# Performance work log

Hardware: AMD Instinct MI355X
Metric: run time of the kernel (lower is better)

Reference implementation:

```python
import jax, jax.numpy as jnp
import numpy as np
import math

B = 128        # batch (= bipartite matching N)
L = 16         # detector layers (MAX_LAYER)
E = 768        # n_embd
D = E // 2     # RFF target_dim
H = 12         # n_head
HD = E // H    # head_size
NL = 6         # n_layer
SEQ = 12       # tokens after concats: 3+3 -> 6 -> +currentLayer -> 12
MAX_LAYER = L
LN_EPS = 1e-3  # keras LayerNormalization default


def setup_inputs() -> dict:
    key = jax.random.key(0)
    ks = jax.random.split(key, 8)
    inp = {}
    inp["X"] = jax.random.normal(ks[0], (B, L, 3), dtype=jnp.float32) * 50.0
    inp["targets"] = jax.random.normal(ks[1], (B, L, 3), dtype=jnp.float32)
    # RandomFourierFeatures params (random per-call in original; fixed here):
    # x: xmin=-160,xmax=160,n=9*1024 ; y: n=12*512 ; dE: xmin=0,xmax=230,n=2300
    specs = [(-160.0, 160.0, 9 * 1024), (-160.0, 160.0, 12 * 512), (0.0, 230.0, 2300)]
    om, ph = [], []
    for i, (xmin, xmax, n) in enumerate(specs):
        k1, k2 = jax.random.split(jax.random.fold_in(ks[2], i))
        omin = 2.0 * math.pi / (xmax - xmin)
        lo, hi = math.log(omin / n), math.log(omin)
        om.append(jnp.exp(jax.random.uniform(k1, (D,), minval=lo, maxval=hi)))
        ph.append(jax.random.uniform(k2, (D,)))  # B ~ U(0,1)*scale, scale=1
    inp["omegas"] = jnp.stack(om).astype(jnp.float32)  # (3, D)
    inp["phases"] = jnp.stack(ph).astype(jnp.float32)  # (3, D)
    # np.random.permutation per layer-step, fixed here
    inp["perms"] = jnp.stack(
        [jax.random.permutation(jax.random.fold_in(ks[3], i), B) for i in range(L - 1)]
    ).astype(jnp.int32)  # (L-1, B)
    # transformer weights (stacked over layers)
    kk = jax.random.split(ks[4], 16)
    s = 0.02
    inp["Wq"] = jax.random.normal(kk[0], (NL, E, H, HD)) * s
    inp["bq"] = jnp.zeros((NL, H, HD))
    inp["Wk"] = jax.random.normal(kk[1], (NL, E, H, HD)) * s
    inp["bk"] = jnp.zeros((NL, H, HD))
    inp["Wv"] = jax.random.normal(kk[2], (NL, E, H, HD)) * s
    inp["bv"] = jnp.zeros((NL, H, HD))
    inp["Wo"] = jax.random.normal(kk[3], (NL, H, HD, E)) * s
    inp["bo"] = jnp.zeros((NL, E))
    inp["ln1g"] = jnp.ones((NL, E)); inp["ln1b"] = jnp.zeros((NL, E))
    inp["ln2g"] = jnp.ones((NL, E)); inp["ln2b"] = jnp.zeros((NL, E))
    inp["W1"] = jax.random.normal(kk[4], (NL, E, 4 * E)) * s
    inp["b1f"] = jnp.zeros((NL, 4 * E))
    inp["W2"] = jax.random.normal(kk[5], (NL, 4 * E, E)) * s
    inp["b2f"] = jnp.zeros((NL, E))
    inp["lnfg"] = jnp.ones((E,)); inp["lnfb"] = jnp.zeros((E,))
    inp["Wout"] = jax.random.normal(kk[6], (SEQ * E, 3)) * s
    inp["bout"] = jnp.zeros((3,))
    return inp


def _ln(x, g, b):
    mu = jnp.mean(x, -1, keepdims=True)
    v = jnp.var(x, -1, keepdims=True)
    return (x - mu) * jax.lax.rsqrt(v + LN_EPS) * g + b


def _greedy_match(cost):
    """Greedy bipartite matching: sort all NxN costs ascending, assign first-come.
    Returns row_to_col_match_vec (N,) int32."""
    N = cost.shape[0]
    order = jnp.argsort(cost.reshape(-1))

    def step(carry, k):
        row, col = carry
        i = k // N
        j = k % N
        ok = (row[i] == -1) & (col[j] == -1)
        row = row.at[i].set(jnp.where(ok, j, row[i]))
        col = col.at[j].set(jnp.where(ok, i, col[j]))
        return (row, col), None

    init = (jnp.full((N,), -1, jnp.int32), jnp.full((N,), -1, jnp.int32))
    (row, _), _ = jax.lax.scan(step, init, order)
    return row


def _forward(X, targets, omegas, phases, perms, Wq, bq, Wk, bk, Wv, bv, Wo, bo,
             ln1g, ln1b, ln2g, ln2b, W1, b1f, W2, b2f, lnfg, lnfb, Wout, bout):
    # RFF: (B,L,3) -> (B,L,3,D)
    XS = jnp.cos(X[..., None] * omegas[None, None, :, :] + phases[None, None, :, :])
    losses = []
    scale = 1.0 / math.sqrt(HD)
    for lidx in range(1, L):
        xc = XS[:, -lidx]        # (B,3,D)
        xp = XS[:, -lidx - 1]    # (B,3,D)
        x = jnp.concatenate([xc, xp], axis=2)            # (B,3,E)
        y = targets[:, -lidx + 1]                        # (B,3)
        y_prev = jnp.broadcast_to(y[:, :, None], (B, 3, E))
        x = jnp.concatenate([x, y_prev], axis=1)         # (B,6,E)
        cur = jnp.full_like(x, float(MAX_LAYER - lidx))
        x = jnp.concatenate([x, cur], axis=1)            # (B,12,E)
        x = x[perms[lidx - 1]]                           # batch permutation
        for l in range(NL):
            h = _ln(x, ln1g[l], ln1b[l])
            q = jnp.einsum('bse,ehd->bshd', h, Wq[l]) + bq[l]
            k = jnp.einsum('bse,ehd->bshd', h, Wk[l]) + bk[l]
            v = jnp.einsum('bse,ehd->bshd', h, Wv[l]) + bv[l]
            att = jax.nn.softmax(jnp.einsum('bqhd,bkhd->bhqk', q, k) * scale, axis=-1)
            o = jnp.einsum('bhqk,bkhd->bqhd', att, v)
            x = x + (jnp.einsum('bqhd,hde->bqe', o, Wo[l]) + bo[l])
            h = _ln(x, ln2g[l], ln2b[l])
            x = x + (jnp.maximum(h @ W1[l] + b1f[l], 0.0) @ W2[l] + b2f[l])
        x = _ln(x, lnfg, lnfb).reshape(B, SEQ * E)
        logits = x @ Wout + bout                         # (B,3)
        tgt = targets[:, -lidx]                          # (B,3)
        cost = jnp.sqrt(jnp.sum((logits[:, None, :] - tgt[None, :, :]) ** 2, axis=-1) + 1e-12)
        m = _greedy_match(jax.lax.stop_gradient(cost))
        lm = logits[m]                                   # gather per original
        losses.append(jnp.mean((lm - tgt) ** 2))
    return jnp.mean(jnp.stack(losses))


def reference(X, targets, omegas, phases, perms, Wq, bq, Wk, bk, Wv, bv, Wo, bo,
              ln1g, ln1b, ln2g, ln2b, W1, b1f, W2, b2f, lnfg, lnfb, Wout, bout):
    return _forward(X, targets, omegas, phases, perms, Wq, bq, Wk, bk, Wv, bv, Wo, bo,
                    ln1g, ln1b, ln2g, ln2b, W1, b1f, W2, b2f, lnfg, lnfb, Wout, bout)
```

## Files before the change

kernel.cpp:

```cpp
#include <hip/hip_runtime.h>
#include <hip/hip_bf16.h>
#include <math.h>

#define B_   128
#define L_   16
#define E_   768
#define D_   384
#define H_   12
#define HD_  64
#define NL_  6
#define SEQ_ 12
#define CH_  5
#define MTOK (CH_*B_*SEQ_)
#define LN_EPS 0.001f
#define WLS   7077888
#define BQS   2304

typedef __attribute__((ext_vector_type(8))) short bf16x8;
typedef __attribute__((ext_vector_type(4))) float f32x4;

#define GLOAD_LDS16(g, l) \
    __builtin_amdgcn_global_load_lds((__attribute__((address_space(1))) const void*)(g), \
                                     (__attribute__((address_space(3))) void*)(l), 16, 0, 0)

__global__ __launch_bounds__(256) void k_xs(const float* __restrict__ X,
                                            const float* __restrict__ om,
                                            const float* __restrict__ ph,
                                            float* __restrict__ XS) {
    int i = blockIdx.x * 256 + threadIdx.x;
    if (i >= B_*L_*3*D_) return;
    int d  = i % D_;
    int ch = (i / D_) % 3;
    int bt = i / (3*D_);
    XS[i] = cosf(X[bt*3 + ch] * om[ch*D_ + d] + ph[ch*D_ + d]);
}

__global__ __launch_bounds__(256) void k_x0(const float* __restrict__ XS,
                                            const float* __restrict__ targets,
                                            const int* __restrict__ perms,
                                            float* __restrict__ x, int cb) {
    int i = blockIdx.x * 256 + threadIdx.x;
    if (i >= MTOK*E_) return;
    int e   = i % E_;
    int tok = i / E_;
    int s   = tok % SEQ_;
    int bi  = (tok / SEQ_) % B_;
    int c   = tok / (SEQ_*B_);
    int cl  = cb + c;
    int lidx = cl + 1;
    int pb  = perms[cl*B_ + bi];
    float val;
    if (s < 3) {
        int t = (e < D_) ? (L_ - lidx) : (L_ - lidx - 1);
        int d = (e < D_) ? e : (e - D_);
        val = XS[((pb*L_ + t)*3 + s)*D_ + d];
    } else if (s < 6) {
        int t = (17 - lidx) & 15;
        val = targets[(pb*L_ + t)*3 + (s - 3)];
    } else {
        val = (float)(L_ - lidx);
    }
    x[i] = val;
}

__global__ __launch_bounds__(256) void k_ln(const float* __restrict__ x,
                                            const float* __restrict__ g,
                                            const float* __restrict__ b,
                                            __hip_bfloat16* __restrict__ h) {
    int gi = blockIdx.x * 256 + threadIdx.x;
    int tok = gi >> 6, lane = gi & 63;
    const float4* xr = (const float4*)(x + (size_t)tok * E_);
    float4 v0 = xr[lane], v1 = xr[lane + 64], v2 = xr[lane + 128];
    float s = v0.x+v0.y+v0.z+v0.w + v1.x+v1.y+v1.z+v1.w + v2.x+v2.y+v2.z+v2.w;
    #pragma unroll
    for (int o = 32; o > 0; o >>= 1) s += __shfl_xor(s, o, 64);
    float mu = s * (1.0f / E_);
    v0.x-=mu; v0.y-=mu; v0.z-=mu; v0.w-=mu;
    v1.x-=mu; v1.y-=mu; v1.z-=mu; v1.w-=mu;
    v2.x-=mu; v2.y-=mu; v2.z-=mu; v2.w-=mu;
    float q = v0.x*v0.x+v0.y*v0.y+v0.z*v0.z+v0.w*v0.w
            + v1.x*v1.x+v1.y*v1.y+v1.z*v1.z+v1.w*v1.w
            + v2.x*v2.x+v2.y*v2.y+v2.z*v2.z+v2.w*v2.w;
    #pragma unroll
    for (int o = 32; o > 0; o >>= 1) q += __shfl_xor(q, o, 64);
    float rstd = rsqrtf(q * (1.0f / E_) + LN_EPS);
    const float4* g4 = (const float4*)g;
    const float4* b4 = (const float4*)b;
    ushort4* h4 = (ushort4*)(h + (size_t)tok * E_);
    #pragma unroll
    for (int k = 0; k < 3; k++) {
        float4 v = (k == 0) ? v0 : (k == 1) ? v1 : v2;
        float4 gg = g4[lane + k*64], bb = b4[lane + k*64];
        ushort4 o;
        o.x = __bfloat16_as_ushort(__float2bfloat16(v.x * rstd * gg.x + bb.x));
        o.y = __bfloat16_as_ushort(__float2bfloat16(v.y * rstd * gg.y + bb.y));
        o.z = __bfloat16_as_ushort(__float2bfloat16(v.z * rstd * gg.z + bb.z));
        o.w = __bfloat16_as_ushort(__float2bfloat16(v.w * rstd * gg.w + bb.w));
        h4[lane + k*64] = o;
    }
}

__global__ __launch_bounds__(256) void k_cvt(const float* __restrict__ Wq,
                                             const float* __restrict__ Wk,
                                             const float* __restrict__ Wv,
                                             const float* __restrict__ Wo,
                                             const float* __restrict__ W1,
                                             const float* __restrict__ W2,
                                             const float* __restrict__ bq,
                                             const float* __restrict__ bk,
                                             const float* __restrict__ bv,
                                             __hip_bfloat16* __restrict__ wl,
                                             float* __restrict__ bqkv, int l) {
    int bid = blockIdx.x;
    int tid = threadIdx.x;
    if (bid == 6912) {
        for (int i = tid; i < 2304; i += 256) {
            float v = (i < 768) ? bq[l*768 + i] : (i < 1536) ? bk[l*768 + i - 768]
                                                             : bv[l*768 + i - 1536];
            bqkv[i] = v;
        }
        return;
    }
    const float* src; __hip_bfloat16* dst; int K, N, ti, tj;
    if (bid < 1728) {
        int part = bid / 576, idx = bid % 576;
        const float* srcs[3] = {Wq, Wk, Wv};
        src = srcs[part] + (size_t)l*768*768; dst = wl + (size_t)part*768*768;
        K = 768; N = 768; tj = idx % 24; ti = idx / 24;
    } else if (bid < 2304) {
        int idx = bid - 1728;
        src = Wo + (size_t)l*768*768; dst = wl + 1769472;
        K = 768; N = 768; tj = idx % 24; ti = idx / 24;
    } else if (bid < 4608) {
        int idx = bid - 2304;
        src = W1 + (size_t)l*768*3072; dst = wl + 2359296;
        K = 768; N = 3072; tj = idx % 96; ti = idx / 96;
    } else {
        int idx = bid - 4608;
        src = W2 + (size_t)l*3072*768; dst = wl + 4718592;
        K = 3072; N = 768; tj = idx % 24; ti = idx / 24;
    }
    __shared__ float tbuf[32][33];
    int tx = tid & 31, ty = tid >> 5;
    #pragma unroll
    for (int p = 0; p < 4; p++) {
        int k = ti*32 + ty + p*8, n = tj*32 + tx;
        tbuf[ty + p*8][tx] = src[(size_t)k*N + n];
    }
    __syncthreads();
    #pragma unroll
    for (int p = 0; p < 4; p++) {
        int n = tj*32 + ty + p*8, k = ti*32 + tx;
        dst[(size_t)n*K + k] = __float2bfloat16(tbuf[tx][ty + p*8]);
    }
}

template<int BN_>
__global__ __launch_bounds__(256) void k_gemm_t(const __hip_bfloat16* __restrict__ A,
                                                const __hip_bfloat16* __restrict__ Bt,
                                                const float* __restrict__ bias,
                                                void* __restrict__ Cp,
                                                int K, int ldc, int flags) {
    constexpr int NF = BN_ / 32;
    __shared__ __align__(16) char smem[8192 + BN_*64];
    char* As = smem;
    char* Bs = smem + 8192;
    int tid = threadIdx.x;
    int lane = tid & 63;
    int w = tid >> 6;
    int wm = (w >> 1) * 64, wn = (w & 1) * (BN_/2);
    int m0 = blockIdx.y * 128, n0 = blockIdx.x * BN_;

    int u1 = tid, u2 = tid + 256;
    int r1 = u1 >> 2, kg1 = ((u1 & 3) ^ ((r1 >> 1) & 3)) * 8;
    int r2 = u2 >> 2, kg2 = ((u2 & 3) ^ ((r2 >> 1) & 3)) * 8;

    f32x4 acc[4][NF] = {};
    int fr = lane & 15, fkg = lane >> 4;

    for (int k0 = 0; k0 < K; k0 += 32) {
        GLOAD_LDS16(A  + (size_t)(m0 + r1) * K + k0 + kg1, As + u1 * 16);
        GLOAD_LDS16(A  + (size_t)(m0 + r2) * K + k0 + kg2, As + u2 * 16);
        GLOAD_LDS16(Bt + (size_t)(n0 + r1) * K + k0 + kg1, Bs + u1 * 16);
        if (BN_ == 128)
            GLOAD_LDS16(Bt + (size_t)(n0 + r2) * K + k0 + kg2, Bs + u2 * 16);
        __syncthreads();
        bf16x8 a[4], b[NF];
        #pragma unroll
        for (int i = 0; i < 4; i++) {
            int m = wm + i*16 + fr;
            a[i] = *(const bf16x8*)(As + m*64 + ((fkg ^ ((m >> 1) & 3)) * 16));
        }
        #pragma unroll
        for (int j = 0; j < NF; j++) {
            int n = wn + j*16 + fr;
            b[j] = *(const bf16x8*)(Bs + n*64 + ((fkg ^ ((n >> 1) & 3)) * 16));
        }
        #pragma unroll
        for (int i = 0; i < 4; i++)
            #pragma unroll
            for (int j = 0; j < NF; j++)
                acc[i][j] = __builtin_amdgcn_mfma_f32_16x16x32_bf16(a[i], b[j], acc[i][j], 0, 0, 0);
        __syncthreads();
    }

    int colL = lane & 15, rowg = (lane >> 4) * 4;
    #pragma unroll
    for (int i = 0; i < 4; i++) {
        #pragma unroll
        for (int j = 0; j < NF; j++) {
            int col = n0 + wn + j*16 + colL;
            float bv = bias ? bias[col] : 0.0f;
            #pragma unroll
            for (int r = 0; r < 4; r++) {
                int row = m0 + wm + i*16 + rowg + r;
                float v = acc[i][j][r] + bv;
                if (flags & 4) v = fmaxf(v, 0.0f);
                size_t off = (size_t)row * ldc + col;
                if (flags & 1)      ((__hip_bfloat16*)Cp)[off] = __float2bfloat16(v);
                else if (flags & 2) ((float*)Cp)[off] += v;
                else                ((float*)Cp)[off] = v;
            }
        }
    }
}

__global__ __launch_bounds__(256) void k_attn(const __hip_bfloat16* __restrict__ qkv,
                                              __hip_bfloat16* __restrict__ o) {
    __shared__ float qs[SEQ_][HD_], ks[SEQ_][HD_], vs[SEQ_][HD_];
    __shared__ float att[SEQ_][SEQ_];
    int blk = blockIdx.x;
    int hh  = blk % H_;
    int cbb = blk / H_;
    int t = threadIdx.x;
    for (int i = t; i < SEQ_*HD_; i += 256) {
        int s = i / HD_, d = i % HD_;
        size_t g = (size_t)(cbb*SEQ_ + s) * 2304 + hh*64 + d;
        qs[s][d] = __bfloat162float(qkv[g]);
        ks[s][d] = __bfloat162float(qkv[g + 768]);
        vs[s][d] = __bfloat162float(qkv[g + 1536]);
    }
    __syncthreads();
    if (t < SEQ_*SEQ_) {
        int qi = t / SEQ_, kj = t % SEQ_;
        float s = 0.f;
        #pragma unroll
        for (int d = 0; d < HD_; d++) s += qs[qi][d] * ks[kj][d];
        att[qi][kj] = s * 0.125f;
    }
    __syncthreads();
    if (t < SEQ_) {
        float mx = -1e30f;
        #pragma unroll
        for (int j = 0; j < SEQ_; j++) mx = fmaxf(mx, att[t][j]);
        float e[SEQ_]; float sum = 0.f;
        #pragma unroll
        for (int j = 0; j < SEQ_; j++) { e[j] = expf(att[t][j] - mx); sum += e[j]; }
        float inv = 1.f / sum;
        #pragma unroll
        for (int j = 0; j < SEQ_; j++) att[t][j] = e[j] * inv;
    }
    __syncthreads();
    for (int i = t; i < SEQ_*HD_; i += 256) {
        int s = i / HD_, d = i % HD_;
        float acc = 0.f;
        #pragma unroll
        for (int j = 0; j < SEQ_; j++) acc += att[s][j] * vs[j][d];
        o[(size_t)(cbb*SEQ_ + s) * 768 + hh*64 + d] = __float2bfloat16(acc);
    }
}

__global__ __launch_bounds__(256) void k_logits(const __hip_bfloat16* __restrict__ hfin,
                                                const float* __restrict__ Wout,
                                                const float* __restrict__ bout,
                                                float* __restrict__ logits, int cb) {
    __shared__ float red[3][256];
    int blk = blockIdx.x;
    int t = threadIdx.x;
    const __hip_bfloat16* row = hfin + (size_t)blk * SEQ_ * E_;
    float a0 = 0.f, a1 = 0.f, a2 = 0.f;
    for (int e = t; e < SEQ_*E_; e += 256) {
        float x = __bfloat162float(row[e]);
        a0 += x * Wout[e*3 + 0]; a1 += x * Wout[e*3 + 1]; a2 += x * Wout[e*3 + 2];
    }
    red[0][t] = a0; red[1][t] = a1; red[2][t] = a2;
    __syncthreads();
    for (int o = 128; o > 0; o >>= 1) {
        if (t < o) { red[0][t] += red[0][t+o]; red[1][t] += red[1][t+o]; red[2][t] += red[2][t+o]; }
        __syncthreads();
    }
    if (t < 3) logits[((size_t)cb*B_ + blk)*3 + t] = red[t][0] + bout[t];
}

__global__ __launch_bounds__(256) void k_cost(const float* __restrict__ logits,
                                              const float* __restrict__ targets,
                                              float* __restrict__ cost) {
    int i = blockIdx.x * 256 + threadIdx.x;
    if (i >= 15*B_*B_) return;
    int j  = i & 127;
    int r  = (i >> 7) & 127;
    int cl = i >> 14;
    int lidx = cl + 1;
    const float* lg = &logits[(cl*B_ + r) * 3];
    const float* tg = &targets[((size_t)j*L_ + (L_ - lidx)) * 3];
    float d0 = lg[0]-tg[0], d1 = lg[1]-tg[1], d2 = lg[2]-tg[2];
    cost[i] = sqrtf(d0*d0 + d1*d1 + d2*d2 + 1e-12f);
}

__global__ __launch_bounds__(1024) void k_match(const float* __restrict__ cost,
                                                const float* __restrict__ logits,
                                                const float* __restrict__ targets,
                                                float* __restrict__ losses) {
    __shared__ unsigned long long wred[16];
    __shared__ int mrow[B_];
    __shared__ unsigned int winner;
    __shared__ float lred[B_];
    int cl = blockIdx.x, t = threadIdx.x;
    const float* cst = cost + (size_t)cl * B_ * B_;
    unsigned long long key[16];
    #pragma unroll
    for (int n = 0; n < 16; n++) {
        unsigned e = n * 1024 + t;
        key[n] = ((unsigned long long)__float_as_uint(cst[e]) << 32) | e;
    }
    int lane = t & 63, w = t >> 6;
    for (int it = 0; it < B_; it++) {
        unsigned long long best = ~0ull;
        #pragma unroll
        for (int n = 0; n < 16; n++) best = key[n] < best ? key[n] : best;
        #pragma unroll
        for (int o = 32; o > 0; o >>= 1) {
            unsigned long long other = __shfl_down(best, o, 64);
            best = other < best ? other : best;
        }
        if (lane == 0) wred[w] = best;
        __syncthreads();
        if (t == 0) {
            unsigned long long b = wred[0];
            #pragma unroll
            for (int q = 1; q < 16; q++) if (wred[q] < b) b = wred[q];
            unsigned e = (unsigned)b;
            winner = e;
            mrow[(e >> 7) & 127] = e & 127;
        }
        __syncthreads();
        unsigned e = winner;
        unsigned wi = (e >> 7) & 127, wj = e & 127;
        #pragma unroll
        for (int n = 0; n < 16; n++) {
            unsigned ke = (unsigned)key[n];
            bool dead = (((ke >> 7) & 127) == wi) | ((ke & 127) == wj);
            key[n] = dead ? ~0ull : key[n];
        }
        __syncthreads();
    }
    int lidx = cl + 1;
    if (t < B_) {
        const float* lg = &logits[(cl*B_ + mrow[t]) * 3];
        const float* tg = &targets[((size_t)t*L_ + (L_ - lidx)) * 3];
        float d0 = lg[0]-tg[0], d1 = lg[1]-tg[1], d2 = lg[2]-tg[2];
        lred[t] = d0*d0 + d1*d1 + d2*d2;
    }
    __syncthreads();
    for (int o = 64; o > 0; o >>= 1) {
        if (t < o) lred[t] += lred[t+o];
        __syncthreads();
    }
    if (t == 0) losses[cl] = lred[0] * (1.0f / (B_*3));
}

__global__ void k_final(const float* __restrict__ losses, float* __restrict__ out) {
    float s = 0.f;
    for (int i = 0; i < 15; i++) s += losses[i];
    out[0] = s * (1.0f / 15.0f);
}

extern "C" void kernel_launch(void* const* d_in, const int* in_sizes, int n_in,
                              void* d_out, int out_size, void* d_ws, size_t ws_size,
                              hipStream_t stream) {
    (void)in_sizes; (void)n_in; (void)out_size;
    const float* X       = (const float*)d_in[0];
    const float* targets = (const float*)d_in[1];
    const float* omegas  = (const float*)d_in[2];
    const float* phases  = (const float*)d_in[3];
    const int*   perms   = (const int*)d_in[4];
    const float* Wq  = (const float*)d_in[5];
    const float* bq  = (const float*)d_in[6];
    const float* Wk  = (const float*)d_in[7];
    const float* bk  = (const float*)d_in[8];
    const float* Wv  = (const float*)d_in[9];
    const float* bv  = (const float*)d_in[10];
    const float* Wo  = (const float*)d_in[11];
    const float* bo  = (const float*)d_in[12];
    const float* ln1g = (const float*)d_in[13];
    const float* ln1b = (const float*)d_in[14];
    const float* ln2g = (const float*)d_in[15];
    const float* ln2b = (const float*)d_in[16];
    const float* W1  = (const float*)d_in[17];
    const float* b1f = (const float*)d_in[18];
    const float* W2  = (const float*)d_in[19];
    const float* b2f = (const float*)d_in[20];
    const float* lnfg = (const float*)d_in[21];
    const float* lnfb = (const float*)d_in[22];
    const float* Wout = (const float*)d_in[23];
    const float* bout = (const float*)d_in[24];

    bool big = ws_size >= 179000000ull;

    char* wsb = (char*)d_ws;
    size_t off = 0;
    auto alloc = [&](size_t bytes) {
        char* p = wsb + off;
        off += (bytes + 255) & ~(size_t)255;
        return p;
    };
    float*          XS     = (float*)alloc(9437184);
    float*          x      = (float*)alloc(23592960);
    __hip_bfloat16* h      = (__hip_bfloat16*)alloc(11796480);
    __hip_bfloat16* qkvh   = (__hip_bfloat16*)alloc(47185920);
    __hip_bfloat16* wl     = (__hip_bfloat16*)alloc(big ? (size_t)6*WLS*2 : (size_t)WLS*2);
    float*          bqkv   = (float*)alloc(big ? 6*BQS*4 : BQS*4);
    float*          logits = (float*)alloc(23040);
    float*          costb  = (float*)alloc(983040);
    float*          losses = (float*)alloc(64);

    k_xs<<<(B_*L_*3*D_ + 255)/256, 256, 0, stream>>>(X, omegas, phases, XS);

    if (big) {
        for (int l = 0; l < NL_; l++)
            k_cvt<<<6913, 256, 0, stream>>>(Wq, Wk, Wv, Wo, W1, W2, bq, bk, bv,
                                            wl + (size_t)l*WLS, bqkv + l*BQS, l);
    }

    dim3 gQKV(2304/128, MTOK/128);
    dim3 gF1 (3072/128, MTOK/128);
    dim3 gO64(768/64,   MTOK/128);
    dim3 gLN (MTOK/4);

    for (int cb = 0; cb < 15; cb += CH_) {
        k_x0<<<(MTOK*E_ + 255)/256, 256, 0, stream>>>(XS, targets, perms, x, cb);
        for (int l = 0; l < NL_; l++) {
            __hip_bfloat16* wlp = big ? wl + (size_t)l*WLS : wl;
            float*          bqp = big ? bqkv + l*BQS : bqkv;
            if (!big)
                k_cvt<<<6913, 256, 0, stream>>>(Wq, Wk, Wv, Wo, W1, W2, bq, bk, bv, wlp, bqp, l);
            k_ln<<<gLN, 256, 0, stream>>>(x, ln1g + l*E_, ln1b + l*E_, h);
            k_gemm_t<128><<<gQKV, 256, 0, stream>>>(h, wlp, bqp, qkvh, 768, 2304, 1);
            k_attn<<<CH_*B_*H_, 256, 0, stream>>>(qkvh, h);
            k_gemm_t<64><<<gO64, 256, 0, stream>>>(h, wlp + 1769472, bo + l*E_, x, 768, 768, 2);
            k_ln<<<gLN, 256, 0, stream>>>(x, ln2g + l*E_, ln2b + l*E_, h);
            k_gemm_t<128><<<gF1, 256, 0, stream>>>(h, wlp + 2359296, b1f + l*3072, qkvh, 768, 3072, 1|4);
            k_gemm_t<64><<<gO64, 256, 0, stream>>>(qkvh, wlp + 4718592, b2f + l*E_, x, 3072, 768, 2);
        }
        k_ln<<<gLN, 256, 0, stream>>>(x, lnfg, lnfb, h);
        k_logits<<<CH_*B_, 256, 0, stream>>>(h, Wout, bout, logits, cb);
    }
    k_cost<<<(15*B_*B_ + 255)/256, 256, 0, stream>>>(logits, targets, costb);
    k_match<<<15, 1024, 0, stream>>>(costb, logits, targets, losses);
    k_final<<<1, 1, 0, stream>>>(losses, (float*)d_out);
}
```

Before: 5.516 ms.

## Process all layers in one chunk, split FFN, rewrite matching as single-wave

Picks chunk size from the workspace size, so all 15 layer-steps are batched into one pass when memory allows, and converts all weight layers in a single launch. The output GEMMs move from 64-wide to 128-wide tiles with a leading-dimension parameter. The FFN is split into two halves of 1536 columns so the intermediate buffer fits in the QKV buffer. The cost and greedy-match kernels are merged into one single-wave kernel that caches per-row minima in LDS and rescans only rows whose minimum was removed. This cuts launch count and per-pass overhead, at the cost of more workspace memory and halved grids for the output GEMMs.

```diff
diff --git a/kernel.cpp b/kernel.cpp
--- a/kernel.cpp
+++ b/kernel.cpp
@@ -10,14 +10,13 @@
 #define HD_  64
 #define NL_  6
 #define SEQ_ 12
-#define CH_  5
-#define MTOK (CH_*B_*SEQ_)
 #define LN_EPS 0.001f
 #define WLS   7077888
 #define BQS   2304
 
 typedef __attribute__((ext_vector_type(8))) short bf16x8;
 typedef __attribute__((ext_vector_type(4))) float f32x4;
+typedef unsigned long long u64;
 
 #define GLOAD_LDS16(g, l) \
     __builtin_amdgcn_global_load_lds((__attribute__((address_space(1))) const void*)(g), \
@@ -38,9 +37,9 @@
 __global__ __launch_bounds__(256) void k_x0(const float* __restrict__ XS,
                                             const float* __restrict__ targets,
                                             const int* __restrict__ perms,
-                                            float* __restrict__ x, int cb) {
+                                            float* __restrict__ x, int cb, int ntok) {
     int i = blockIdx.x * 256 + threadIdx.x;
-    if (i >= MTOK*E_) return;
+    if (i >= ntok*E_) return;
     int e   = i % E_;
     int tok = i / E_;
     int s   = tok % SEQ_;
@@ -109,9 +108,13 @@
                                              const float* __restrict__ bq,
                                              const float* __restrict__ bk,
                                              const float* __restrict__ bv,
-                                             __hip_bfloat16* __restrict__ wl,
-                                             float* __restrict__ bqkv, int l) {
+                                             __hip_bfloat16* __restrict__ wl0,
+                                             float* __restrict__ bqkv0, int lbase) {
     int bid = blockIdx.x;
+    int l   = lbase + bid / 6913;
+    bid %= 6913;
+    __hip_bfloat16* wl = wl0 + (size_t)(l - lbase) * WLS;
+    float* bqkv = bqkv0 + (l - lbase) * BQS;
     int tid = threadIdx.x;
     if (bid == 6912) {
         for (int i = tid; i < 2304; i += 256) {
@@ -155,51 +158,45 @@
     }
 }
 
-template<int BN_>
-__global__ __launch_bounds__(256) void k_gemm_t(const __hip_bfloat16* __restrict__ A,
-                                                const __hip_bfloat16* __restrict__ Bt,
-                                                const float* __restrict__ bias,
-                                                void* __restrict__ Cp,
-                                                int K, int ldc, int flags) {
-    constexpr int NF = BN_ / 32;
-    __shared__ __align__(16) char smem[8192 + BN_*64];
+__global__ __launch_bounds__(256) void k_gemm(const __hip_bfloat16* __restrict__ A,
+                                              const __hip_bfloat16* __restrict__ Bt,
+                                              const float* __restrict__ bias,
+                                              void* __restrict__ Cp,
+                                              int K, int ldb, int ldc, int flags) {
+    __shared__ __align__(16) char smem[16384];
     char* As = smem;
     char* Bs = smem + 8192;
     int tid = threadIdx.x;
     int lane = tid & 63;
     int w = tid >> 6;
-    int wm = (w >> 1) * 64, wn = (w & 1) * (BN_/2);
-    int m0 = blockIdx.y * 128, n0 = blockIdx.x * BN_;
+    int wm = (w >> 1) * 64, wn = (w & 1) * 64;
+    int m0 = blockIdx.y * 128, n0 = blockIdx.x * 128;
 
     int u1 = tid, u2 = tid + 256;
     int r1 = u1 >> 2, kg1 = ((u1 & 3) ^ ((r1 >> 1) & 3)) * 8;
     int r2 = u2 >> 2, kg2 = ((u2 & 3) ^ ((r2 >> 1) & 3)) * 8;
 
-    f32x4 acc[4][NF] = {};
+    f32x4 acc[4][4] = {};
     int fr = lane & 15, fkg = lane >> 4;
 
     for (int k0 = 0; k0 < K; k0 += 32) {
-        GLOAD_LDS16(A  + (size_t)(m0 + r1) * K + k0 + kg1, As + u1 * 16);
-        GLOAD_LDS16(A  + (size_t)(m0 + r2) * K + k0 + kg2, As + u2 * 16);
-        GLOAD_LDS16(Bt + (size_t)(n0 + r1) * K + k0 + kg1, Bs + u1 * 16);
-        if (BN_ == 128)
-            GLOAD_LDS16(Bt + (size_t)(n0 + r2) * K + k0 + kg2, Bs + u2 * 16);
+        GLOAD_LDS16(A  + (size_t)(m0 + r1) * K   + k0 + kg1, As + u1 * 16);
+        GLOAD_LDS16(A  + (size_t)(m0 + r2) * K   + k0 + kg2, As + u2 * 16);
+        GLOAD_LDS16(Bt + (size_t)(n0 + r1) * ldb + k0 + kg1, Bs + u1 * 16);
+        GLOAD_LDS16(Bt + (size_t)(n0 + r2) * ldb + k0 + kg2, Bs + u2 * 16);
         __syncthreads();
-        bf16x8 a[4], b[NF];
+        bf16x8 a[4], b[4];
         #pragma unroll
         for (int i = 0; i < 4; i++) {
             int m = wm + i*16 + fr;
             a[i] = *(const bf16x8*)(As + m*64 + ((fkg ^ ((m >> 1) & 3)) * 16));
-        }
-        #pragma unroll
-        for (int j = 0; j < NF; j++) {
-            int n = wn + j*16 + fr;
-            b[j] = *(const bf16x8*)(Bs + n*64 + ((fkg ^ ((n >> 1) & 3)) * 16));
+            int n = wn + i*16 + fr;
+            b[i] = *(const bf16x8*)(Bs + n*64 + ((fkg ^ ((n >> 1) & 3)) * 16));
         }
         #pragma unroll
         for (int i = 0; i < 4; i++)
             #pragma unroll
-            for (int j = 0; j < NF; j++)
+            for (int j = 0; j < 4; j++)
                 acc[i][j] = __builtin_amdgcn_mfma_f32_16x16x32_bf16(a[i], b[j], acc[i][j], 0, 0, 0);
         __syncthreads();
     }
@@ -208,7 +205,7 @@
     #pragma unroll
     for (int i = 0; i < 4; i++) {
         #pragma unroll
-        for (int j = 0; j < NF; j++) {
+        for (int j = 0; j < 4; j++) {
             int col = n0 + wn + j*16 + colL;
             float bv = bias ? bias[col] : 0.0f;
             #pragma unroll
@@ -292,81 +289,72 @@
     if (t < 3) logits[((size_t)cb*B_ + blk)*3 + t] = red[t][0] + bout[t];
 }
 
-__global__ __launch_bounds__(256) void k_cost(const float* __restrict__ logits,
+__global__ __launch_bounds__(64) void k_match(const float* __restrict__ logits,
                                               const float* __restrict__ targets,
-                                              float* __restrict__ cost) {
-    int i = blockIdx.x * 256 + threadIdx.x;
-    if (i >= 15*B_*B_) return;
-    int j  = i & 127;
-    int r  = (i >> 7) & 127;
-    int cl = i >> 14;
+                                              float* __restrict__ losses) {
+    __shared__ float cst[128 * 129];
+    __shared__ float tg[128][3];
+    __shared__ int mrow[128];
+    int cl = blockIdx.x, lane = threadIdx.x;
     int lidx = cl + 1;
-    const float* lg = &logits[(cl*B_ + r) * 3];
-    const float* tg = &targets[((size_t)j*L_ + (L_ - lidx)) * 3];
-    float d0 = lg[0]-tg[0], d1 = lg[1]-tg[1], d2 = lg[2]-tg[2];
-    cost[i] = sqrtf(d0*d0 + d1*d1 + d2*d2 + 1e-12f);
-}
-
-__global__ __launch_bounds__(1024) void k_match(const float* __restrict__ cost,
-                                                const float* __restrict__ logits,
-                                                const float* __restrict__ targets,
-                                                float* __restrict__ losses) {
-    __shared__ unsigned long long wred[16];
-    __shared__ int mrow[B_];
-    __shared__ unsigned int winner;
-    __shared__ float lred[B_];
-    int cl = blockIdx.x, t = threadIdx.x;
-    const float* cst = cost + (size_t)cl * B_ * B_;
-    unsigned long long key[16];
-    #pragma unroll
-    for (int n = 0; n < 16; n++) {
-        unsigned e = n * 1024 + t;
-        key[n] = ((unsigned long long)__float_as_uint(cst[e]) << 32) | e;
-    }
-    int lane = t & 63, w = t >> 6;
-    for (int it = 0; it < B_; it++) {
-        unsigned long long best = ~0ull;
-        #pragma unroll
-        for (int n = 0; n < 16; n++) best = key[n] < best ? key[n] : best;
+    for (int j = lane; j < 128; j += 64) {
+        const float* t = &targets[((size_t)j*L_ + (L_ - lidx)) * 3];
+        tg[j][0] = t[0]; tg[j][1] = t[1]; tg[j][2] = t[2];
+    }
+    __syncthreads();
+    u64 rowBest[2];
+    #pragma unroll
+    for (int hh = 0; hh < 2; hh++) {
+        int r = lane + hh*64;
+        const float* lg = &logits[(cl*B_ + r) * 3];
+        float l0 = lg[0], l1 = lg[1], l2 = lg[2];
+        u64 best = ~0ull;
+        for (int c = 0; c < 128; c++) {
+            float d0 = l0 - tg[c][0], d1 = l1 - tg[c][1], d2 = l2 - tg[c][2];
+            float cost = sqrtf(d0*d0 + d1*d1 + d2*d2 + 1e-12f);
+            cst[r*129 + c] = cost;
+            u64 key = ((u64)__float_as_uint(cost) << 32) | (unsigned)(r*128 + c);
+            best = key < best ? key : best;
+        }
+        rowBest[hh] = best;
+    }
+    for (int it = 0; it < 128; it++) {
+        u64 b = rowBest[0] < rowBest[1] ? rowBest[0] : rowBest[1];
         #pragma unroll
         for (int o = 32; o > 0; o >>= 1) {
-            unsigned long long other = __shfl_down(best, o, 64);
-            best = other < best ? other : best;
-        }
-        if (lane == 0) wred[w] = best;
-        __syncthreads();
-        if (t == 0) {
-            unsigned long long b = wred[0];
-            #pragma unroll
-            for (int q = 1; q < 16; q++) if (wred[q] < b) b = wred[q];
-            unsigned e = (unsigned)b;
-            winner = e;
-            mrow[(e >> 7) & 127] = e & 127;
-        }
-        __syncthreads();
-        unsigned e = winner;
-        unsigned wi = (e >> 7) & 127, wj = e & 127;
-        #pragma unroll
-        for (int n = 0; n < 16; n++) {
-            unsigned ke = (unsigned)key[n];
-            bool dead = (((ke >> 7) & 127) == wi) | ((ke & 127) == wj);
-            key[n] = dead ? ~0ull : key[n];
-        }
-        __syncthreads();
-    }
-    int lidx = cl + 1;
-    if (t < B_) {
-        const float* lg = &logits[(cl*B_ + mrow[t]) * 3];
-        const float* tg = &targets[((size_t)t*L_ + (L_ - lidx)) * 3];
-        float d0 = lg[0]-tg[0], d1 = lg[1]-tg[1], d2 = lg[2]-tg[2];
-        lred[t] = d0*d0 + d1*d1 + d2*d2;
-    }
-    __syncthreads();
-    for (int o = 64; o > 0; o >>= 1) {
-        if (t < o) lred[t] += lred[t+o];
-        __syncthreads();
-    }
-    if (t == 0) losses[cl] = lred[0] * (1.0f / (B_*3));
+            u64 other = __shfl_xor(b, o, 64);
+            b = other < b ? other : b;
+        }
+        unsigned wi = ((unsigned)b >> 7) & 127, wj = (unsigned)b & 127;
+        if (lane == 0) mrow[wi] = wj;
+        #pragma unroll
+        for (int hh = 0; hh < 2; hh++) {
+            int r = lane + hh*64;
+            if ((unsigned)r == wi) rowBest[hh] = ~0ull;
+            cst[r*129 + wj] = 1e30f;
+            if (rowBest[hh] != ~0ull && ((unsigned)rowBest[hh] & 127) == wj) {
+                u64 best = ~0ull;
+                for (int c = 0; c < 128; c++) {
+                    u64 key = ((u64)__float_as_uint(cst[r*129 + c]) << 32)
+                              | (unsigned)(r*128 + c);
+                    best = key < best ? key : best;
+                }
+                rowBest[hh] = best;
+            }
+        }
+    }
+    __syncthreads();
+    float a = 0.f;
+    #pragma unroll
+    for (int hh = 0; hh < 2; hh++) {
+        int r = lane + hh*64;
+        const float* lg = &logits[(cl*B_ + mrow[r]) * 3];
+        float d0 = lg[0]-tg[r][0], d1 = lg[1]-tg[r][1], d2 = lg[2]-tg[r][2];
+        a += d0*d0 + d1*d1 + d2*d2;
+    }
+    #pragma unroll
+    for (int o = 32; o > 0; o >>= 1) a += __shfl_xor(a, o, 64);
+    if (lane == 0) losses[cl] = a * (1.0f / (B_*3));
 }
 
 __global__ void k_final(const float* __restrict__ losses, float* __restrict__ out) {
@@ -405,7 +393,9 @@
     const float* Wout = (const float*)d_in[23];
     const float* bout = (const float*)d_in[24];
 
-    bool big = ws_size >= 179000000ull;
+    int  CL    = (ws_size >= 306800000ull) ? 15 : 5;
+    bool hoist = (CL == 15) || (ws_size >= 165300000ull);
+    int  M     = CL * B_ * SEQ_;
 
     char* wsb = (char*)d_ws;
     size_t off = 0;
@@ -415,47 +405,47 @@
         return p;
     };
     float*          XS     = (float*)alloc(9437184);
-    float*          x      = (float*)alloc(23592960);
-    __hip_bfloat16* h      = (__hip_bfloat16*)alloc(11796480);
-    __hip_bfloat16* qkvh   = (__hip_bfloat16*)alloc(47185920);
-    __hip_bfloat16* wl     = (__hip_bfloat16*)alloc(big ? (size_t)6*WLS*2 : (size_t)WLS*2);
-    float*          bqkv   = (float*)alloc(big ? 6*BQS*4 : BQS*4);
+    float*          x      = (float*)alloc((size_t)M*E_*4);
+    __hip_bfloat16* h      = (__hip_bfloat16*)alloc((size_t)M*E_*2);
+    __hip_bfloat16* qkvh   = (__hip_bfloat16*)alloc((size_t)M*2304*2);
+    __hip_bfloat16* wl     = (__hip_bfloat16*)alloc((hoist ? 6 : 1) * (size_t)WLS*2);
+    float*          bqkv   = (float*)alloc((hoist ? 6 : 1) * (size_t)BQS*4);
     float*          logits = (float*)alloc(23040);
-    float*          costb  = (float*)alloc(983040);
     float*          losses = (float*)alloc(64);
 
     k_xs<<<(B_*L_*3*D_ + 255)/256, 256, 0, stream>>>(X, omegas, phases, XS);
 
-    if (big) {
-        for (int l = 0; l < NL_; l++)
-            k_cvt<<<6913, 256, 0, stream>>>(Wq, Wk, Wv, Wo, W1, W2, bq, bk, bv,
-                                            wl + (size_t)l*WLS, bqkv + l*BQS, l);
-    }
-
-    dim3 gQKV(2304/128, MTOK/128);
-    dim3 gF1 (3072/128, MTOK/128);
-    dim3 gO64(768/64,   MTOK/128);
-    dim3 gLN (MTOK/4);
-
-    for (int cb = 0; cb < 15; cb += CH_) {
-        k_x0<<<(MTOK*E_ + 255)/256, 256, 0, stream>>>(XS, targets, perms, x, cb);
+    if (hoist)
+        k_cvt<<<6*6913, 256, 0, stream>>>(Wq, Wk, Wv, Wo, W1, W2, bq, bk, bv, wl, bqkv, 0);
+
+    dim3 gQKV(2304/128, M/128);
+    dim3 gO  (768/128,  M/128);
+    dim3 gF1 (1536/128, M/128);
+    dim3 gLN (M/4);
+
+    for (int cb = 0; cb < 15; cb += CL) {
+        k_x0<<<(M*E_)/256, 256, 0, stream>>>(XS, targets, perms, x, cb, M);
         for (int l = 0; l < NL_; l++) {
-            __hip_bfloat16* wlp = big ? wl + (size_t)l*WLS : wl;
-            float*          bqp = big ? bqkv + l*BQS : bqkv;
-            if (!big)
+            __hip_bfloat16* wlp = hoist ? wl + (size_t)l*WLS : wl;
+            float*          bqp = hoist ? bqkv + l*BQS : bqkv;
+            if (!hoist)
                 k_cvt<<<6913, 256, 0, stream>>>(Wq, Wk, Wv, Wo, W1, W2, bq, bk, bv, wlp, bqp, l);
             k_ln<<<gLN, 256, 0, stream>>>(x, ln1g + l*E_, ln1b + l*E_, h);
-            k_gemm_t<128><<<gQKV, 256, 0, stream>>>(h, wlp, bqp, qkvh, 768, 2304, 1);
-            k_attn<<<CH_*B_*H_, 256, 0, stream>>>(qkvh, h);
-            k_gemm_t<64><<<gO64, 256, 0, stream>>>(h, wlp + 1769472, bo + l*E_, x, 768, 768, 2);
+            k_gemm<<<gQKV, 256, 0, stream>>>(h, wlp, bqp, qkvh, 768, 768, 2304, 1);
+            k_attn<<<CL*B_*H_, 256, 0, stream>>>(qkvh, h);
+            k_gemm<<<gO, 256, 0, stream>>>(h, wlp + 1769472, bo + l*E_, x, 768, 768, 768, 2);
             k_ln<<<gLN, 256, 0, stream>>>(x, ln2g + l*E_, ln2b + l*E_, h);
-            k_gemm_t<128><<<gF1, 256, 0, stream>>>(h, wlp + 2359296, b1f + l*3072, qkvh, 768, 3072, 1|4);
-            k_gemm_t<64><<<gO64, 256, 0, stream>>>(qkvh, wlp + 4718592, b2f + l*E_, x, 3072, 768, 2);
+            for (int nc = 0; nc < 2; nc++) {
+                k_gemm<<<gF1, 256, 0, stream>>>(h, wlp + 2359296 + (size_t)nc*1536*768,
+                                                b1f + l*3072 + nc*1536, qkvh, 768, 768, 1536, 1|4);
+                k_gemm<<<gO, 256, 0, stream>>>(qkvh, wlp + 4718592 + (size_t)nc*1536,
+                                               nc == 0 ? (b2f + l*E_) : (const float*)nullptr,
+                                               x, 1536, 3072, 768, 2);
+            }
         }
         k_ln<<<gLN, 256, 0, stream>>>(x, lnfg, lnfb, h);
-        k_logits<<<CH_*B_, 256, 0, stream>>>(h, Wout, bout, logits, cb);
-    }
-    k_cost<<<(15*B_*B_ + 255)/256, 256, 0, stream>>>(logits, targets, costb);
-    k_match<<<15, 1024, 0, stream>>>(costb, logits, targets, losses);
+        k_logits<<<CL*B_, 256, 0, stream>>>(h, Wout, bout, logits, cb);
+    }
+    k_match<<<15, 64, 0, stream>>>(logits, targets, losses);
     k_final<<<1, 1, 0, stream>>>(losses, (float*)d_out);
 }
```

After: 6.922 ms. 1.25x slower.
